# Kernel optimization log

Measured on AMD Instinct MI355X. Metric: run time of the kernel, lower is better.

The kernel has to match this reference:

```python
import jax, jax.numpy as jnp
import numpy as np

T, B = 256, 64
X_DIM, H_DIM, Z_DIM = 128, 1024, 128


def _lin(k, out_d, in_d):
    return jax.random.normal(k, (out_d, in_d), jnp.float32) * 0.05


def setup_inputs() -> dict:
    key = jax.random.key(0)
    ks = jax.random.split(key, 18)
    return {
        "x": jax.random.normal(ks[0], (T, B, X_DIM), jnp.float32),
        "y": jax.random.uniform(ks[1], (T, B, X_DIM), jnp.float32),
        "eps": jax.random.normal(ks[2], (T, B, Z_DIM), jnp.float32),
        # hidden_state_rnn: GRU(x_dim -> h_dim), bias=False
        "h_Wih": _lin(ks[3], 3 * H_DIM, X_DIM),
        "h_Whh": _lin(ks[4], 3 * H_DIM, H_DIM),
        # rnn: GRU(h_dim + x_dim -> h_dim), bias=False (input is [y_t, h_t])
        "a_Wih": _lin(ks[5], 3 * H_DIM, X_DIM + H_DIM),
        "a_Whh": _lin(ks[6], 3 * H_DIM, H_DIM),
        "enc_W1": _lin(ks[7], H_DIM, H_DIM), "enc_b1": jnp.zeros(H_DIM, jnp.float32),
        "enc_W2": _lin(ks[8], H_DIM, H_DIM), "enc_b2": jnp.zeros(H_DIM, jnp.float32),
        "encm_W": _lin(ks[9], Z_DIM, H_DIM), "encm_b": jnp.zeros(Z_DIM, jnp.float32),
        "encs_W": _lin(ks[10], Z_DIM, H_DIM), "encs_b": jnp.zeros(Z_DIM, jnp.float32),
        "pr_W": _lin(ks[11], H_DIM, H_DIM), "pr_b": jnp.zeros(H_DIM, jnp.float32),
        "prm_W": _lin(ks[12], Z_DIM, H_DIM), "prm_b": jnp.zeros(Z_DIM, jnp.float32),
        "prs_W": _lin(ks[13], Z_DIM, H_DIM), "prs_b": jnp.zeros(Z_DIM, jnp.float32),
        "dec_W1": _lin(ks[14], H_DIM, H_DIM + Z_DIM), "dec_b1": jnp.zeros(H_DIM, jnp.float32),
        "dec_W2": _lin(ks[15], H_DIM, H_DIM), "dec_b2": jnp.zeros(H_DIM, jnp.float32),
        "decm_W": _lin(ks[16], X_DIM, H_DIM), "decm_b": jnp.zeros(X_DIM, jnp.float32),
        "decs_W": _lin(ks[17], X_DIM, H_DIM), "decs_b": jnp.zeros(X_DIM, jnp.float32),
    }


def _gru(xs, Wih, Whh):
    """Single-layer PyTorch-style GRU without biases. xs: [T,B,in]. Returns [T,B,H]."""
    h0 = jnp.zeros((xs.shape[1], Whh.shape[1]), xs.dtype)
    def step(h, xt):
        gi = xt @ Wih.T                      # [B, 3H]
        gh = h @ Whh.T                       # [B, 3H]
        ir, iz, inn = jnp.split(gi, 3, axis=-1)
        hr, hz, hn = jnp.split(gh, 3, axis=-1)
        r = jax.nn.sigmoid(ir + hr)
        zg = jax.nn.sigmoid(iz + hz)
        n = jnp.tanh(inn + r * hn)
        h_new = (1.0 - zg) * n + zg * h
        return h_new, h_new
    return jax.lax.scan(step, h0, xs)[1]


def srnn_forward(x, y, eps, h_Wih, h_Whh, a_Wih, a_Whh,
                 enc_W1, enc_b1, enc_W2, enc_b2, encm_W, encm_b, encs_W, encs_b,
                 pr_W, pr_b, prm_W, prm_b, prs_W, prs_b,
                 dec_W1, dec_b1, dec_W2, dec_b2, decm_W, decm_b, decs_W, decs_b):
    h_seq = _gru(x, h_Wih, h_Whh)            # [T,B,H] forward-time states
    # NOTE: original code aliases h_list and reverses it in place, so all later
    # uses of h_list[t] actually see the time-reversed sequence. Reproduce that.
    h_rev = h_seq[::-1]
    y_rev = y[::-1]
    a_rev = _gru(jnp.concatenate([y_rev, h_rev], axis=-1), a_Wih, a_Whh)  # backward GRU
    a_fwd = a_rev[::-1]                      # a at forward time t saw steps t..T-1

    enc = jax.nn.relu(jax.nn.relu(a_fwd @ enc_W1.T + enc_b1) @ enc_W2.T + enc_b2)
    enc_mean = enc @ encm_W.T + encm_b       # [T,B,Z]
    enc_std = jax.nn.softplus(enc @ encs_W.T + encs_b)
    z = eps * enc_std + enc_mean             # reparameterized sample

    pri = jax.nn.relu(h_rev @ pr_W.T + pr_b)  # bug-faithful: reversed h
    prior_mean = pri @ prm_W.T + prm_b
    prior_std = jax.nn.softplus(pri @ prs_W.T + prs_b)

    dec = jax.nn.relu(
        jax.nn.relu(jnp.concatenate([z, h_rev], axis=-1) @ dec_W1.T + dec_b1)
        @ dec_W2.T + dec_b2)
    dec_mean = jax.nn.sigmoid(dec @ decm_W.T + decm_b)  # [T,B,X]
    dec_std = jax.nn.softplus(dec @ decs_W.T + decs_b)

    kld = 0.5 * jnp.sum(
        2.0 * jnp.log(prior_std) - 2.0 * jnp.log(enc_std)
        + (enc_std ** 2 + (enc_mean - prior_mean) ** 2) / prior_std ** 2 - 1.0)
    nll = -jnp.sum(y * jnp.log(dec_mean) + (1.0 - y) * jnp.log(1.0 - dec_mean))
    return kld, nll, enc_mean, enc_std, dec_mean, dec_std


def reference(x, y, eps, h_Wih, h_Whh, a_Wih, a_Whh,
              enc_W1, enc_b1, enc_W2, enc_b2, encm_W, encm_b, encs_W, encs_b,
              pr_W, pr_b, prm_W, prm_b, prs_W, prs_b,
              dec_W1, dec_b1, dec_W2, dec_b2, decm_W, decm_b, decs_W, decs_b):
    return srnn_forward(x, y, eps, h_Wih, h_Whh, a_Wih, a_Whh,
                        enc_W1, enc_b1, enc_W2, enc_b2, encm_W, encm_b, encs_W, encs_b,
                        pr_W, pr_b, prm_W, prm_b, prs_W, prs_b,
                        dec_W1, dec_b1, dec_W2, dec_b2, decm_W, decm_b, decs_W, decs_b)
```

## Files before the change

### kernel.cpp

```cpp
#include <hip/hip_runtime.h>
#include <cstdint>
#include <cstddef>

#define NT   256
#define NB   64
#define XD   128
#define HD   1024
#define ZD   128
#define H3   3072
#define TBM  16384

typedef __attribute__((ext_vector_type(8))) short bf16x8;
typedef __attribute__((ext_vector_type(4))) float f32x4;
typedef __attribute__((ext_vector_type(4))) unsigned int u32x4;

__device__ __forceinline__ unsigned short f2bf(float f){
  unsigned int u = __float_as_uint(f);
  u += 0x7fffu + ((u >> 16) & 1u);
  return (unsigned short)(u >> 16);
}
__device__ __forceinline__ float bf2f(unsigned short h){
  return __uint_as_float(((unsigned int)h) << 16);
}

template<int N>
__device__ __forceinline__ void vwait(){
  asm volatile("s_waitcnt vmcnt(%0)" :: "i"(N) : "memory");
  __builtin_amdgcn_sched_barrier(0);
}

__device__ __forceinline__ float fsigmoid(float x){
  return 1.f / (1.f + __expf(-x));
}
__device__ __forceinline__ float ftanh(float x){
  float xc = fminf(fmaxf(x, -15.f), 15.f);
  float e = __expf(2.f * xc);
  return (e - 1.f) / (e + 1.f);
}

__device__ __forceinline__ void wait_tags(const unsigned int* tags, unsigned int target){
  if (threadIdx.x < 64){
    const unsigned int* p = tags + threadIdx.x * 32;
    unsigned int a, b;
    asm volatile("global_load_dword %0, %2, off sc0 sc1\n\t"
                 "global_load_dword %1, %2, off sc0 sc1"
                 : "=v"(a), "=v"(b) : "v"(p) : "memory");
    for (;;){
      asm volatile("s_waitcnt vmcnt(1)" ::: "memory");
      __builtin_amdgcn_sched_barrier(0);
      if (__all((int)(a >= target))) break;
      asm volatile("global_load_dword %0, %1, off sc0 sc1" : "=v"(a) : "v"(p) : "memory");
      asm volatile("s_waitcnt vmcnt(1)" ::: "memory");
      __builtin_amdgcn_sched_barrier(0);
      if (__all((int)(b >= target))) break;
      asm volatile("global_load_dword %0, %1, off sc0 sc1" : "=v"(b) : "v"(p) : "memory");
    }
    asm volatile("s_waitcnt vmcnt(0)" ::: "memory");
    __builtin_amdgcn_sched_barrier(0);
  }
  __syncthreads();
}

struct CvtArgs { const float* src[17]; };

__global__ void cvt_all(CvtArgs a, unsigned short* wdst, unsigned short* xdst, unsigned short* ydst){
  const long NG = 2572288;
  for (long g = blockIdx.x*blockDim.x + threadIdx.x; g < NG; g += (long)gridDim.x*blockDim.x){
    long i = g * 8;
    const float* s; unsigned short* d;
    if      (i < 393216)  { s=a.src[0]+i;             d=wdst+i; }
    else if (i < 3538944) { s=a.src[1]+(i-393216);    d=wdst+i; }
    else if (i < 7077888) { s=a.src[2]+(i-3538944);   d=wdst+i; }
    else if (i < 10223616){ s=a.src[3]+(i-7077888);   d=wdst+i; }
    else if (i < 11272192){ s=a.src[4]+(i-10223616);  d=wdst+i; }
    else if (i < 12320768){ s=a.src[5]+(i-11272192);  d=wdst+i; }
    else if (i < 12451840){ s=a.src[6]+(i-12320768);  d=wdst+i; }
    else if (i < 12582912){ s=a.src[7]+(i-12451840);  d=wdst+i; }
    else if (i < 13631488){ s=a.src[8]+(i-12582912);  d=wdst+i; }
    else if (i < 13762560){ s=a.src[9]+(i-13631488);  d=wdst+i; }
    else if (i < 13893632){ s=a.src[10]+(i-13762560); d=wdst+i; }
    else if (i < 15073280){ s=a.src[11]+(i-13893632); d=wdst+i; }
    else if (i < 16121856){ s=a.src[12]+(i-15073280); d=wdst+i; }
    else if (i < 16252928){ s=a.src[13]+(i-16121856); d=wdst+i; }
    else if (i < 16384000){ s=a.src[14]+(i-16252928); d=wdst+i; }
    else if (i < 18481152){ s=a.src[15]+(i-16384000); d=xdst+(i-16384000); }
    else                  { s=a.src[16]+(i-18481152); d=ydst+(i-18481152); }
    float4 v0 = *(const float4*)s;
    float4 v1 = *(const float4*)(s + 4);
    u32x4 o;
    o.x = (unsigned int)f2bf(v0.x) | ((unsigned int)f2bf(v0.y) << 16);
    o.y = (unsigned int)f2bf(v0.z) | ((unsigned int)f2bf(v0.w) << 16);
    o.z = (unsigned int)f2bf(v1.x) | ((unsigned int)f2bf(v1.y) << 16);
    o.w = (unsigned int)f2bf(v1.z) | ((unsigned int)f2bf(v1.w) << 16);
    *(u32x4*)d = o;
  }
}

template<int ACT, int OUT_BF, int BIAS>
__launch_bounds__(256)
__global__ void gemm_bf16(const unsigned short* __restrict__ A1, int rev1, int K1,
                          const unsigned short* __restrict__ A2, int rev2, int K,
                          const unsigned short* __restrict__ W,
                          const float* __restrict__ bias,
                          void* __restrict__ Cv, int N, int m0)
{
  __shared__ __align__(16) unsigned short As[128][40];
  __shared__ __align__(16) unsigned short Ws[128][40];
  const int tid   = threadIdx.x;
  const int mbase = blockIdx.y * 128;
  const int nbase = blockIdx.x * 128;
  const int wid = tid >> 6, lane = tid & 63;
  const int wr = wid >> 1, wc = wid & 1;
  const int fr = lane & 15;
  const int kc = (lane >> 4) * 8;
  const int K2 = K - K1;
  const int nk = K >> 5;

  f32x4 acc[4][4];
  #pragma unroll
  for (int i = 0; i < 4; ++i)
    #pragma unroll
    for (int j = 0; j < 4; ++j)
      acc[i][j] = (f32x4){0.f, 0.f, 0.f, 0.f};

  for (int ks = 0; ks < nk; ++ks){
    const int k0 = ks << 5;
    __syncthreads();
    for (int l = tid; l < 512; l += 256){
      int row = l >> 2, c = l & 3;
      int kk = k0 + c*8;
      int m = m0 + mbase + row;
      uint4 v;
      if (kk < K1){
        int mm = rev1 ? (((255 - (m >> 6)) << 6) | (m & 63)) : m;
        v = *(const uint4*)(A1 + (size_t)mm * K1 + kk);
      } else {
        int mm = rev2 ? (((255 - (m >> 6)) << 6) | (m & 63)) : m;
        v = *(const uint4*)(A2 + (size_t)mm * K2 + (kk - K1));
      }
      *(uint4*)&As[row][c*8] = v;
    }
    for (int l = tid; l < 512; l += 256){
      int row = l >> 2, c = l & 3;
      uint4 v = *(const uint4*)(W + (size_t)(nbase + row) * K + k0 + c*8);
      *(uint4*)&Ws[row][c*8] = v;
    }
    __syncthreads();
    bf16x8 af[4], bfm[4];
    #pragma unroll
    for (int f = 0; f < 4; ++f) af[f]  = *(const bf16x8*)&As[wr*64 + f*16 + fr][kc];
    #pragma unroll
    for (int f = 0; f < 4; ++f) bfm[f] = *(const bf16x8*)&Ws[wc*64 + f*16 + fr][kc];
    #pragma unroll
    for (int i = 0; i < 4; ++i)
      #pragma unroll
      for (int j = 0; j < 4; ++j)
        acc[i][j] = __builtin_amdgcn_mfma_f32_16x16x32_bf16(af[i], bfm[j], acc[i][j], 0, 0, 0);
  }

  #pragma unroll
  for (int i = 0; i < 4; ++i){
    #pragma unroll
    for (int j = 0; j < 4; ++j){
      #pragma unroll
      for (int r = 0; r < 4; ++r){
        int row = mbase + wr*64 + i*16 + (lane >> 4)*4 + r;
        int col = nbase + wc*64 + j*16 + fr;
        float v = acc[i][j][r];
        if (BIAS) v += bias[col];
        if (ACT == 1) v = fmaxf(v, 0.f);
        else if (ACT == 2) v = 1.f / (1.f + expf(-v));
        else if (ACT == 3) v = (v > 20.f) ? v : log1pf(expf(v));
        if (OUT_BF) ((unsigned short*)Cv)[(size_t)row * N + col] = f2bf(v);
        else        ((float*)Cv)[(size_t)row * N + col] = v;
      }
    }
  }
}

template<int ACTA, int ACTB>
__launch_bounds__(256)
__global__ void gemm_dual(const unsigned short* __restrict__ A,
                          const unsigned short* __restrict__ Wa, const float* __restrict__ ba,
                          float* __restrict__ Ca,
                          const unsigned short* __restrict__ Wb, const float* __restrict__ bb,
                          float* __restrict__ Cb)
{
  const unsigned short* W = blockIdx.x ? Wb : Wa;
  const float* bias = blockIdx.x ? bb : ba;
  float* C = blockIdx.x ? Cb : Ca;
  const int act = blockIdx.x ? ACTB : ACTA;

  __shared__ __align__(16) unsigned short As[128][40];
  __shared__ __align__(16) unsigned short Ws[128][40];
  const int tid   = threadIdx.x;
  const int mbase = blockIdx.y * 128;
  const int wid = tid >> 6, lane = tid & 63;
  const int wr = wid >> 1, wc = wid & 1;
  const int fr = lane & 15;
  const int kc = (lane >> 4) * 8;

  f32x4 acc[4][4];
  #pragma unroll
  for (int i = 0; i < 4; ++i)
    #pragma unroll
    for (int j = 0; j < 4; ++j)
      acc[i][j] = (f32x4){0.f, 0.f, 0.f, 0.f};

  for (int ks = 0; ks < 32; ++ks){
    const int k0 = ks << 5;
    __syncthreads();
    for (int l = tid; l < 512; l += 256){
      int row = l >> 2, c = l & 3;
      *(uint4*)&As[row][c*8] = *(const uint4*)(A + (size_t)(mbase + row) * HD + k0 + c*8);
    }
    for (int l = tid; l < 512; l += 256){
      int row = l >> 2, c = l & 3;
      *(uint4*)&Ws[row][c*8] = *(const uint4*)(W + (size_t)row * HD + k0 + c*8);
    }
    __syncthreads();
    bf16x8 af[4], bfm[4];
    #pragma unroll
    for (int f = 0; f < 4; ++f) af[f]  = *(const bf16x8*)&As[wr*64 + f*16 + fr][kc];
    #pragma unroll
    for (int f = 0; f < 4; ++f) bfm[f] = *(const bf16x8*)&Ws[wc*64 + f*16 + fr][kc];
    #pragma unroll
    for (int i = 0; i < 4; ++i)
      #pragma unroll
      for (int j = 0; j < 4; ++j)
        acc[i][j] = __builtin_amdgcn_mfma_f32_16x16x32_bf16(af[i], bfm[j], acc[i][j], 0, 0, 0);
  }

  #pragma unroll
  for (int i = 0; i < 4; ++i){
    #pragma unroll
    for (int j = 0; j < 4; ++j){
      #pragma unroll
      for (int r = 0; r < 4; ++r){
        int row = mbase + wr*64 + i*16 + (lane >> 4)*4 + r;
        int col = wc*64 + j*16 + fr;
        float v = acc[i][j][r] + bias[col];
        if (act == 1) v = fmaxf(v, 0.f);
        else if (act == 2) v = 1.f / (1.f + expf(-v));
        else if (act == 3) v = (v > 20.f) ? v : log1pf(expf(v));
        C[(size_t)row * ZD + col] = v;
      }
    }
  }
}

__device__ void gemm_gi_tile(char* smem,
                             const unsigned short* __restrict__ A1, int rev1, int K1,
                             const unsigned short* __restrict__ A2, int rev2, int K,
                             const unsigned short* __restrict__ W,
                             unsigned short* __restrict__ C, int m0, int bx, int by)
{
  unsigned short (*As)[40] = (unsigned short(*)[40])smem;
  unsigned short (*Ws)[40] = (unsigned short(*)[40])(smem + 10240);
  const int tid   = threadIdx.x;
  const int mbase = by * 128;
  const int nbase = bx * 128;
  const int wid = tid >> 6, lane = tid & 63;
  const int wr = wid >> 1, wc = wid & 1;
  const int fr = lane & 15;
  const int kc = (lane >> 4) * 8;
  const int K2 = K - K1;
  const int nk = K >> 5;

  f32x4 acc[4][4];
  #pragma unroll
  for (int i = 0; i < 4; ++i)
    #pragma unroll
    for (int j = 0; j < 4; ++j)
      acc[i][j] = (f32x4){0.f, 0.f, 0.f, 0.f};

  for (int ks = 0; ks < nk; ++ks){
    const int k0 = ks << 5;
    __syncthreads();
    for (int l = tid; l < 512; l += 256){
      int row = l >> 2, c = l & 3;
      int kk = k0 + c*8;
      int m = m0 + mbase + row;
      uint4 v;
      if (kk < K1){
        int mm = rev1 ? (((255 - (m >> 6)) << 6) | (m & 63)) : m;
        v = *(const uint4*)(A1 + (size_t)mm * K1 + kk);
      } else {
        int mm = rev2 ? (((255 - (m >> 6)) << 6) | (m & 63)) : m;
        v = *(const uint4*)(A2 + (size_t)mm * K2 + (kk - K1));
      }
      *(uint4*)&As[row][c*8] = v;
    }
    for (int l = tid; l < 512; l += 256){
      int row = l >> 2, c = l & 3;
      uint4 v = *(const uint4*)(W + (size_t)(nbase + row) * K + k0 + c*8);
      *(uint4*)&Ws[row][c*8] = v;
    }
    __syncthreads();
    bf16x8 af[4], bfm[4];
    #pragma unroll
    for (int f = 0; f < 4; ++f) af[f]  = *(const bf16x8*)&As[wr*64 + f*16 + fr][kc];
    #pragma unroll
    for (int f = 0; f < 4; ++f) bfm[f] = *(const bf16x8*)&Ws[wc*64 + f*16 + fr][kc];
    #pragma unroll
    for (int i = 0; i < 4; ++i)
      #pragma unroll
      for (int j = 0; j < 4; ++j)
        acc[i][j] = __builtin_amdgcn_mfma_f32_16x16x32_bf16(af[i], bfm[j], acc[i][j], 0, 0, 0);
  }

  #pragma unroll
  for (int i = 0; i < 4; ++i){
    #pragma unroll
    for (int j = 0; j < 4; ++j){
      #pragma unroll
      for (int r = 0; r < 4; ++r){
        int row = mbase + wr*64 + i*16 + (lane >> 4)*4 + r;
        int col = nbase + wc*64 + j*16 + fr;
        C[(size_t)row * H3 + col] = f2bf(acc[i][j][r]);
      }
    }
  }
  __syncthreads();
}

__device__ void gru_body(char* smem,
                         const unsigned short* __restrict__ W3,
                         const unsigned short* __restrict__ gi,
                         unsigned short* __restrict__ seq,
                         float* __restrict__ hstate,
                         unsigned int* __restrict__ tags,
                         int t0, int dir, int out_off, int nsteps)
{
  uint4 (*Wf)[3][64] = (uint4(*)[3][64])smem;
  unsigned short (*hb2)[16] = (unsigned short(*)[16])(smem + 98304);
  const int tid  = threadIdx.x;
  const int bid  = blockIdx.x;
  const int c0   = bid * 16;
  const int wid  = tid >> 6, lane = tid & 63;
  const int fr   = lane & 15, q = lane >> 4;
  const int rowb = wid*16 + q*4;
  const int arow = wid*16 + fr;

  for (int ks = wid*8; ks < wid*8 + 8; ++ks)
    #pragma unroll
    for (int g = 0; g < 3; ++g)
      Wf[ks][g][lane] = *(const uint4*)(W3 + (size_t)(g*HD + c0 + fr)*HD + ks*32 + q*8);

  float hc[4];
  if (t0 == 0){
    hc[0] = hc[1] = hc[2] = hc[3] = 0.f;
  } else {
    #pragma unroll
    for (int r = 0; r < 4; ++r)
      hc[r] = hstate[(size_t)(rowb + r)*HD + c0 + fr];
  }
  __syncthreads();

  for (int tt = 0; tt < nsteps; ++tt){
    const int t = t0 + tt;

    unsigned short g_ir[4], g_iz[4], g_in[4];
    {
      const unsigned short* gb = gi + (size_t)tt*NB*H3;
      #pragma unroll
      for (int r = 0; r < 4; ++r){
        const unsigned short* p = gb + (size_t)(rowb + r)*H3 + c0 + fr;
        g_ir[r] = p[0];
        g_iz[r] = p[HD];
        g_in[r] = p[2*HD];
      }
    }

    f32x4 aR = (f32x4){0.f,0.f,0.f,0.f};
    f32x4 aZ = (f32x4){0.f,0.f,0.f,0.f};
    f32x4 aN = (f32x4){0.f,0.f,0.f,0.f};

    if (t > 0){
      if (tt >= 1) wait_tags(tags, (unsigned int)tt);
      const unsigned short* hp = seq + (size_t)(out_off + dir*(t-1))*NB*HD
                                     + (size_t)arow*HD + q*8;
      u32x4 A[32];
      #pragma unroll
      for (int ks = 0; ks < 32; ++ks)
        asm volatile("global_load_dwordx4 %0, %1, off offset:%2"
                     : "=v"(A[ks]) : "v"(hp), "i"(ks*64));
      #pragma unroll
      for (int b4 = 0; b4 < 4; ++b4){
        if (b4 == 0) vwait<24>();
        else if (b4 == 1) vwait<16>();
        else if (b4 == 2) vwait<8>();
        else vwait<0>();
        #pragma unroll
        for (int k8 = 0; k8 < 8; ++k8){
          const int ks = b4*8 + k8;
          bf16x8 a = *(const bf16x8*)&A[ks];
          aR = __builtin_amdgcn_mfma_f32_16x16x32_bf16(a, *(const bf16x8*)&Wf[ks][0][lane], aR, 0, 0, 0);
          aZ = __builtin_amdgcn_mfma_f32_16x16x32_bf16(a, *(const bf16x8*)&Wf[ks][1][lane], aZ, 0, 0, 0);
          aN = __builtin_amdgcn_mfma_f32_16x16x32_bf16(a, *(const bf16x8*)&Wf[ks][2][lane], aN, 0, 0, 0);
        }
      }
    }

    #pragma unroll
    for (int r = 0; r < 4; ++r){
      float rr = fsigmoid(bf2f(g_ir[r]) + aR[r]);
      float zz = fsigmoid(bf2f(g_iz[r]) + aZ[r]);
      float nn = ftanh(bf2f(g_in[r]) + rr * aN[r]);
      hc[r] = (1.f - zz) * nn + zz * hc[r];
      hb2[rowb + r][fr] = f2bf(hc[r]);
    }
    __syncthreads();
    {
      int row = tid >> 2, c4 = (tid & 3) * 4;
      unsigned long long v = *(const unsigned long long*)&hb2[row][c4];
      unsigned long long* dst = (unsigned long long*)(seq + (size_t)(out_off + dir*t)*NB*HD
                                                          + (size_t)row*HD + c0 + c4);
      (void)__hip_atomic_exchange(dst, v, __ATOMIC_RELAXED, __HIP_MEMORY_SCOPE_AGENT);
    }
    if (tt < nsteps - 1){
      vwait<0>();
      __syncthreads();
      if (tid == 0)
        (void)__hip_atomic_exchange(tags + bid*32, (unsigned int)(tt + 1),
                                    __ATOMIC_RELAXED, __HIP_MEMORY_SCOPE_AGENT);
    }
  }

  #pragma unroll
  for (int r = 0; r < 4; ++r)
    hstate[(size_t)(rowb + r)*HD + c0 + fr] = hc[r];
}

__global__ __launch_bounds__(256, 1)
void gru_seq(const unsigned short* __restrict__ W3, const unsigned short* __restrict__ gi,
             unsigned short* __restrict__ seq, float* __restrict__ hstate,
             unsigned int* __restrict__ tags, int t0, int dir, int out_off, int nsteps)
{
  __shared__ __align__(16) char smem[100608];
  gru_body(smem, W3, gi, seq, hstate, tags, t0, dir, out_off, nsteps);
}

__global__ __launch_bounds__(256, 1)
void gru_fat(const unsigned short* __restrict__ W3, const unsigned short* __restrict__ gi,
             unsigned short* __restrict__ seq, float* __restrict__ hstate,
             unsigned int* __restrict__ tags, int t0, int dir, int out_off, int nsteps,
             const unsigned short* __restrict__ gA1, int grev1, int gK1,
             const unsigned short* __restrict__ gA2, int grev2, int gK,
             const unsigned short* __restrict__ gW, unsigned short* __restrict__ gC, int gm0)
{
  __shared__ __align__(16) char smem[100608];
  if (blockIdx.x < 64){
    gru_body(smem, W3, gi, seq, hstate, tags, t0, dir, out_off, nsteps);
  } else {
    for (int tl = blockIdx.x - 64; tl < 768; tl += 96)
      gemm_gi_tile(smem, gA1, grev1, gK1, gA2, grev2, gK, gW, gC, gm0, tl % 24, tl / 24);
  }
}

__global__ void z_make(const float* __restrict__ eps, const float* __restrict__ em,
                       const float* __restrict__ es, unsigned short* __restrict__ zb, int n){
  for (int i = blockIdx.x*blockDim.x + threadIdx.x; i < n; i += gridDim.x*blockDim.x)
    zb[i] = f2bf(eps[i] * es[i] + em[i]);
}

__global__ void kld_partial(const float* __restrict__ em, const float* __restrict__ es,
                            const float* __restrict__ pm, const float* __restrict__ ps,
                            float* __restrict__ part, int n){
  float s = 0.f;
  for (int i = blockIdx.x*blockDim.x + threadIdx.x; i < n; i += gridDim.x*blockDim.x){
    float e = es[i], p = ps[i], d = em[i] - pm[i];
    s += 2.f*(logf(p) - logf(e)) + (e*e + d*d)/(p*p) - 1.f;
  }
  __shared__ float red[256];
  red[threadIdx.x] = s; __syncthreads();
  for (int off = 128; off; off >>= 1){
    if (threadIdx.x < off) red[threadIdx.x] += red[threadIdx.x + off];
    __syncthreads();
  }
  if (threadIdx.x == 0) part[blockIdx.x] = red[0];
}

__global__ void nll_partial(const float* __restrict__ y, const float* __restrict__ dm,
                            float* __restrict__ part, int n){
  float s = 0.f;
  for (int i = blockIdx.x*blockDim.x + threadIdx.x; i < n; i += gridDim.x*blockDim.x){
    float yy = y[i], d = dm[i];
    s += yy * logf(d) + (1.f - yy) * logf(1.f - d);
  }
  __shared__ float red[256];
  red[threadIdx.x] = s; __syncthreads();
  for (int off = 128; off; off >>= 1){
    if (threadIdx.x < off) red[threadIdx.x] += red[threadIdx.x + off];
    __syncthreads();
  }
  if (threadIdx.x == 0) part[blockIdx.x] = red[0];
}

__global__ void final_sum(const float* __restrict__ part, int n, float scale, float* __restrict__ out){
  float s = 0.f;
  for (int i = threadIdx.x; i < n; i += 256) s += part[i];
  __shared__ float red[256];
  red[threadIdx.x] = s; __syncthreads();
  for (int off = 128; off; off >>= 1){
    if (threadIdx.x < off) red[threadIdx.x] += red[threadIdx.x + off];
    __syncthreads();
  }
  if (threadIdx.x == 0) out[0] = scale * red[0];
}

extern "C" void kernel_launch(void* const* d_in, const int* in_sizes, int n_in,
                              void* d_out, int out_size, void* d_ws, size_t ws_size,
                              hipStream_t stream)
{
  const float* y   = (const float*)d_in[1];
  const float* eps = (const float*)d_in[2];
  const float* enc_b1 = (const float*)d_in[8];
  const float* enc_b2 = (const float*)d_in[10];
  const float* encm_b = (const float*)d_in[12];
  const float* encs_b = (const float*)d_in[14];
  const float* pr_b   = (const float*)d_in[16];
  const float* prm_b  = (const float*)d_in[18];
  const float* prs_b  = (const float*)d_in[20];
  const float* dec_b1 = (const float*)d_in[22];
  const float* dec_b2 = (const float*)d_in[24];
  const float* decm_b = (const float*)d_in[26];
  const float* decs_b = (const float*)d_in[28];

  char* ws = (char*)d_ws;
  size_t off = 0;
  auto alloc = [&](size_t bytes){ size_t o = off; off += (bytes + 255) & ~(size_t)255; return o; };
  const size_t o_big   = alloc((size_t)71303168);
  const size_t o_hseq  = alloc((size_t)TBM * HD * 2);
  const size_t o_aseq  = alloc((size_t)TBM * HD * 2);
  const size_t o_wbf   = alloc((size_t)16384000 * 2);
  const size_t o_hst   = alloc((size_t)NB * HD * 4);
  const size_t o_bar   = alloc((size_t)65536);
  const size_t o_pkld  = alloc((size_t)1024 * 4);
  const size_t o_pnll  = alloc((size_t)1024 * 4);
  (void)off; (void)ws_size;

  char* big = ws + o_big;
  unsigned short* gihA = (unsigned short*)(big);
  unsigned short* gihB = (unsigned short*)(big + 25165824);
  unsigned short* xbf  = (unsigned short*)(big + 50331648);
  unsigned short* ybf  = (unsigned short*)(big + 54525952);
  unsigned short* tA  = (unsigned short*)(big);
  unsigned short* tB  = (unsigned short*)(big + 33554432);
  unsigned short* zbf = (unsigned short*)(big + 67108864);

  unsigned short* hseq = (unsigned short*)(ws + o_hseq);
  unsigned short* aseq = (unsigned short*)(ws + o_aseq);
  unsigned short* wbf  = (unsigned short*)(ws + o_wbf);
  float* hstate = (float*)(ws + o_hst);
  unsigned int* bar = (unsigned int*)(ws + o_bar);
  float* pkld = (float*)(ws + o_pkld);
  float* pnll = (float*)(ws + o_pnll);

  const int widx[15] = {3,4,5,6,7,9,11,13,15,17,19,21,23,25,27};
  const size_t wsz[15] = {393216,3145728,3538944,3145728,1048576,1048576,131072,131072,
                          1048576,131072,131072,1179648,1048576,131072,131072};
  size_t woff[15]; { size_t a = 0; for (int i = 0; i < 15; ++i){ woff[i] = a; a += wsz[i]; } }
  unsigned short* w_hWih = wbf + woff[0];
  unsigned short* w_hWhh = wbf + woff[1];
  unsigned short* w_aWih = wbf + woff[2];
  unsigned short* w_aWhh = wbf + woff[3];
  unsigned short* w_enc1 = wbf + woff[4];
  unsigned short* w_enc2 = wbf + woff[5];
  unsigned short* w_encm = wbf + woff[6];
  unsigned short* w_encs = wbf + woff[7];
  unsigned short* w_pr   = wbf + woff[8];
  unsigned short* w_prm  = wbf + woff[9];
  unsigned short* w_prs  = wbf + woff[10];
  unsigned short* w_dec1 = wbf + woff[11];
  unsigned short* w_dec2 = wbf + woff[12];
  unsigned short* w_decm = wbf + woff[13];
  unsigned short* w_decs = wbf + woff[14];

  float* out = (float*)d_out;
  float* em_out = out + 2;
  float* es_out = out + 2 + 2097152;
  float* dm_out = out + 2 + 2*2097152;
  float* ds_out = out + 2 + 3*2097152;
  float* pm = dm_out;
  float* ps = ds_out;

  CvtArgs ca;
  for (int i = 0; i < 15; ++i) ca.src[i] = (const float*)d_in[widx[i]];
  ca.src[15] = (const float*)d_in[0];
  ca.src[16] = (const float*)d_in[1];
  cvt_all<<<2048, 256, 0, stream>>>(ca, wbf, xbf, ybf);
  (void)hipMemsetAsync(bar, 0, 65536, stream);

  const dim3 blk(256);
  const dim3 gQ3072(24, 32);
  const dim3 g1024(HD/128, TBM/128);
  const dim3 gDual(2, TBM/128);
  const unsigned short* nul = (const unsigned short*)nullptr;

  gemm_bf16<0,1,0><<<gQ3072, blk, 0, stream>>>(xbf, 0, XD, nul, 0, XD, w_hWih, nullptr, gihA, H3, 0);
  gru_fat<<<160, blk, 0, stream>>>(w_hWhh, gihA, hseq, hstate, bar + 0*2048, 0,   +1, 0, 64,
                                   xbf, 0, XD, nul, 0, XD, w_hWih, gihB, 4096);
  gru_fat<<<160, blk, 0, stream>>>(w_hWhh, gihB, hseq, hstate, bar + 1*2048, 64,  +1, 0, 64,
                                   xbf, 0, XD, nul, 0, XD, w_hWih, gihA, 8192);
  gru_fat<<<160, blk, 0, stream>>>(w_hWhh, gihA, hseq, hstate, bar + 2*2048, 128, +1, 0, 64,
                                   xbf, 0, XD, nul, 0, XD, w_hWih, gihB, 12288);
  gru_seq<<<64, blk, 0, stream>>>(w_hWhh, gihB, hseq, hstate, bar + 3*2048, 192, +1, 0, 64);

  gemm_bf16<0,1,0><<<gQ3072, blk, 0, stream>>>(ybf, 1, XD, hseq, 1, XD + HD, w_aWih, nullptr, gihA, H3, 0);
  gru_fat<<<160, blk, 0, stream>>>(w_aWhh, gihA, aseq, hstate, bar + 4*2048, 0,   -1, 255, 64,
                                   ybf, 1, XD, hseq, 1, XD + HD, w_aWih, gihB, 4096);
  gru_fat<<<160, blk, 0, stream>>>(w_aWhh, gihB, aseq, hstate, bar + 5*2048, 64,  -1, 255, 64,
                                   ybf, 1, XD, hseq, 1, XD + HD, w_aWih, gihA, 8192);
  gru_fat<<<160, blk, 0, stream>>>(w_aWhh, gihA, aseq, hstate, bar + 6*2048, 128, -1, 255, 64,
                                   ybf, 1, XD, hseq, 1, XD + HD, w_aWih, gihB, 12288);
  gru_seq<<<64, blk, 0, stream>>>(w_aWhh, gihB, aseq, hstate, bar + 7*2048, 192, -1, 255, 64);

  gemm_bf16<1,1,1><<<g1024, blk, 0, stream>>>(aseq, 0, HD, nul, 0, HD, w_enc1, enc_b1, tA, HD, 0);
  gemm_bf16<1,1,1><<<g1024, blk, 0, stream>>>(tA, 0, HD, nul, 0, HD, w_enc2, enc_b2, tB, HD, 0);
  gemm_dual<0,3><<<gDual, blk, 0, stream>>>(tB, w_encm, encm_b, em_out, w_encs, encs_b, es_out);
  z_make<<<2048, 256, 0, stream>>>(eps, em_out, es_out, zbf, TBM*ZD);

  gemm_bf16<1,1,1><<<g1024, blk, 0, stream>>>(hseq, 1, HD, nul, 1, HD, w_pr, pr_b, tA, HD, 0);
  gemm_dual<0,3><<<gDual, blk, 0, stream>>>(tA, w_prm, prm_b, pm, w_prs, prs_b, ps);
  kld_partial<<<1024, 256, 0, stream>>>(em_out, es_out, pm, ps, pkld, TBM*ZD);
  final_sum<<<1, 256, 0, stream>>>(pkld, 1024, 0.5f, out + 0);

  gemm_bf16<1,1,1><<<g1024, blk, 0, stream>>>(zbf, 0, ZD, hseq, 1, ZD + HD, w_dec1, dec_b1, tA, HD, 0);
  gemm_bf16<1,1,1><<<g1024, blk, 0, stream>>>(tA, 0, HD, nul, 0, HD, w_dec2, dec_b2, tB, HD, 0);
  gemm_dual<2,3><<<gDual, blk, 0, stream>>>(tB, w_decm, decm_b, dm_out, w_decs, decs_b, ds_out);

  nll_partial<<<1024, 256, 0, stream>>>(y, dm_out, pnll, TBM*XD);
  final_sum<<<1, 256, 0, stream>>>(pnll, 1024, -1.0f, out + 1);
}
```

Before: 4.633 ms.

## Fuse mean/std head GEMMs with z sampling, KLD and NLL reductions; per-wave barrier tags

```diff
diff --git a/kernel.cpp b/kernel.cpp
--- a/kernel.cpp
+++ b/kernel.cpp
@@ -41,19 +41,19 @@
 __device__ __forceinline__ void wait_tags(const unsigned int* tags, unsigned int target){
   if (threadIdx.x < 64){
     const unsigned int* p = tags + threadIdx.x * 32;
-    unsigned int a, b;
-    asm volatile("global_load_dword %0, %2, off sc0 sc1\n\t"
-                 "global_load_dword %1, %2, off sc0 sc1"
+    u32x4 a, b;
+    asm volatile("global_load_dwordx4 %0, %2, off sc0 sc1\n\t"
+                 "global_load_dwordx4 %1, %2, off sc0 sc1"
                  : "=v"(a), "=v"(b) : "v"(p) : "memory");
     for (;;){
       asm volatile("s_waitcnt vmcnt(1)" ::: "memory");
       __builtin_amdgcn_sched_barrier(0);
-      if (__all((int)(a >= target))) break;
-      asm volatile("global_load_dword %0, %1, off sc0 sc1" : "=v"(a) : "v"(p) : "memory");
+      if (__all((int)(a.x >= target && a.y >= target && a.z >= target && a.w >= target))) break;
+      asm volatile("global_load_dwordx4 %0, %1, off sc0 sc1" : "=v"(a) : "v"(p) : "memory");
       asm volatile("s_waitcnt vmcnt(1)" ::: "memory");
       __builtin_amdgcn_sched_barrier(0);
-      if (__all((int)(b >= target))) break;
-      asm volatile("global_load_dword %0, %1, off sc0 sc1" : "=v"(b) : "v"(p) : "memory");
+      if (__all((int)(b.x >= target && b.y >= target && b.z >= target && b.w >= target))) break;
+      asm volatile("global_load_dwordx4 %0, %1, off sc0 sc1" : "=v"(b) : "v"(p) : "memory");
     }
     asm volatile("s_waitcnt vmcnt(0)" ::: "memory");
     __builtin_amdgcn_sched_barrier(0);
@@ -178,74 +178,105 @@
   }
 }
 
-template<int ACTA, int ACTB>
+template<int MODE>
 __launch_bounds__(256)
-__global__ void gemm_dual(const unsigned short* __restrict__ A,
-                          const unsigned short* __restrict__ Wa, const float* __restrict__ ba,
-                          float* __restrict__ Ca,
-                          const unsigned short* __restrict__ Wb, const float* __restrict__ bb,
-                          float* __restrict__ Cb)
+__global__ void gemm_two(const unsigned short* __restrict__ A,
+                         const unsigned short* __restrict__ Wa, const float* __restrict__ ba,
+                         const unsigned short* __restrict__ Wb, const float* __restrict__ bb,
+                         float* __restrict__ Oa, float* __restrict__ Ob,
+                         const float* __restrict__ aux1, const float* __restrict__ aux2,
+                         unsigned short* __restrict__ zb, float* __restrict__ part)
 {
-  const unsigned short* W = blockIdx.x ? Wb : Wa;
-  const float* bias = blockIdx.x ? bb : ba;
-  float* C = blockIdx.x ? Cb : Ca;
-  const int act = blockIdx.x ? ACTB : ACTA;
-
   __shared__ __align__(16) unsigned short As[128][40];
-  __shared__ __align__(16) unsigned short Ws[128][40];
+  __shared__ __align__(16) unsigned short Wsa[128][40];
+  __shared__ __align__(16) unsigned short Wsb[128][40];
+  __shared__ float red[256];
   const int tid   = threadIdx.x;
-  const int mbase = blockIdx.y * 128;
+  const int mbase = blockIdx.x * 128;
   const int wid = tid >> 6, lane = tid & 63;
   const int wr = wid >> 1, wc = wid & 1;
-  const int fr = lane & 15;
-  const int kc = (lane >> 4) * 8;
-
-  f32x4 acc[4][4];
+  const int fr = lane & 15, q = lane >> 4;
+  const int kc = q * 8;
+
+  f32x4 accA[4][4], accB[4][4];
   #pragma unroll
   for (int i = 0; i < 4; ++i)
     #pragma unroll
-    for (int j = 0; j < 4; ++j)
-      acc[i][j] = (f32x4){0.f, 0.f, 0.f, 0.f};
+    for (int j = 0; j < 4; ++j){
+      accA[i][j] = (f32x4){0.f, 0.f, 0.f, 0.f};
+      accB[i][j] = (f32x4){0.f, 0.f, 0.f, 0.f};
+    }
 
   for (int ks = 0; ks < 32; ++ks){
     const int k0 = ks << 5;
     __syncthreads();
     for (int l = tid; l < 512; l += 256){
       int row = l >> 2, c = l & 3;
-      *(uint4*)&As[row][c*8] = *(const uint4*)(A + (size_t)(mbase + row) * HD + k0 + c*8);
+      *(uint4*)&As[row][c*8]  = *(const uint4*)(A  + (size_t)(mbase + row) * HD + k0 + c*8);
     }
     for (int l = tid; l < 512; l += 256){
       int row = l >> 2, c = l & 3;
-      *(uint4*)&Ws[row][c*8] = *(const uint4*)(W + (size_t)row * HD + k0 + c*8);
-    }
-    __syncthreads();
-    bf16x8 af[4], bfm[4];
-    #pragma unroll
-    for (int f = 0; f < 4; ++f) af[f]  = *(const bf16x8*)&As[wr*64 + f*16 + fr][kc];
-    #pragma unroll
-    for (int f = 0; f < 4; ++f) bfm[f] = *(const bf16x8*)&Ws[wc*64 + f*16 + fr][kc];
+      *(uint4*)&Wsa[row][c*8] = *(const uint4*)(Wa + (size_t)row * HD + k0 + c*8);
+    }
+    for (int l = tid; l < 512; l += 256){
+      int row = l >> 2, c = l & 3;
+      *(uint4*)&Wsb[row][c*8] = *(const uint4*)(Wb + (size_t)row * HD + k0 + c*8);
+    }
+    __syncthreads();
+    bf16x8 af[4], wa[4], wb[4];
+    #pragma unroll
+    for (int f = 0; f < 4; ++f) af[f] = *(const bf16x8*)&As[wr*64 + f*16 + fr][kc];
+    #pragma unroll
+    for (int f = 0; f < 4; ++f) wa[f] = *(const bf16x8*)&Wsa[wc*64 + f*16 + fr][kc];
+    #pragma unroll
+    for (int f = 0; f < 4; ++f) wb[f] = *(const bf16x8*)&Wsb[wc*64 + f*16 + fr][kc];
     #pragma unroll
     for (int i = 0; i < 4; ++i)
       #pragma unroll
-      for (int j = 0; j < 4; ++j)
-        acc[i][j] = __builtin_amdgcn_mfma_f32_16x16x32_bf16(af[i], bfm[j], acc[i][j], 0, 0, 0);
-  }
-
+      for (int j = 0; j < 4; ++j){
+        accA[i][j] = __builtin_amdgcn_mfma_f32_16x16x32_bf16(af[i], wa[j], accA[i][j], 0, 0, 0);
+        accB[i][j] = __builtin_amdgcn_mfma_f32_16x16x32_bf16(af[i], wb[j], accB[i][j], 0, 0, 0);
+      }
+  }
+
+  float s = 0.f;
   #pragma unroll
   for (int i = 0; i < 4; ++i){
     #pragma unroll
     for (int j = 0; j < 4; ++j){
       #pragma unroll
       for (int r = 0; r < 4; ++r){
-        int row = mbase + wr*64 + i*16 + (lane >> 4)*4 + r;
+        int row = mbase + wr*64 + i*16 + q*4 + r;
         int col = wc*64 + j*16 + fr;
-        float v = acc[i][j][r] + bias[col];
-        if (act == 1) v = fmaxf(v, 0.f);
-        else if (act == 2) v = 1.f / (1.f + expf(-v));
-        else if (act == 3) v = (v > 20.f) ? v : log1pf(expf(v));
-        C[(size_t)row * ZD + col] = v;
-      }
-    }
+        size_t idx = (size_t)row * ZD + col;
+        float va = accA[i][j][r] + ba[col];
+        float vb = accB[i][j][r] + bb[col];
+        float sb = (vb > 20.f) ? vb : log1pf(expf(vb));
+        if (MODE == 0){
+          Oa[idx] = va;
+          Ob[idx] = sb;
+          zb[idx] = f2bf(aux1[idx] * sb + va);
+        } else if (MODE == 1){
+          float em = aux1[idx], es = aux2[idx];
+          float d = em - va;
+          s += 2.f*(logf(sb) - logf(es)) + (es*es + d*d)/(sb*sb) - 1.f;
+        } else {
+          float dm = 1.f / (1.f + expf(-va));
+          Oa[idx] = dm;
+          Ob[idx] = sb;
+          float yy = aux1[idx];
+          s += yy * logf(dm) + (1.f - yy) * logf(1.f - dm);
+        }
+      }
+    }
+  }
+  if (MODE != 0){
+    red[tid] = s; __syncthreads();
+    for (int off2 = 128; off2; off2 >>= 1){
+      if (tid < off2) red[tid] += red[tid + off2];
+      __syncthreads();
+    }
+    if (tid == 0) part[blockIdx.x] = red[0];
   }
 }
 
@@ -420,9 +451,8 @@
     }
     if (tt < nsteps - 1){
       vwait<0>();
-      __syncthreads();
-      if (tid == 0)
-        (void)__hip_atomic_exchange(tags + bid*32, (unsigned int)(tt + 1),
+      if (lane == 0)
+        (void)__hip_atomic_exchange(tags + bid*32 + wid, (unsigned int)(tt + 1),
                                     __ATOMIC_RELAXED, __HIP_MEMORY_SCOPE_AGENT);
     }
   }
@@ -456,45 +486,6 @@
     for (int tl = blockIdx.x - 64; tl < 768; tl += 96)
       gemm_gi_tile(smem, gA1, grev1, gK1, gA2, grev2, gK, gW, gC, gm0, tl % 24, tl / 24);
   }
-}
-
-__global__ void z_make(const float* __restrict__ eps, const float* __restrict__ em,
-                       const float* __restrict__ es, unsigned short* __restrict__ zb, int n){
-  for (int i = blockIdx.x*blockDim.x + threadIdx.x; i < n; i += gridDim.x*blockDim.x)
-    zb[i] = f2bf(eps[i] * es[i] + em[i]);
-}
-
-__global__ void kld_partial(const float* __restrict__ em, const float* __restrict__ es,
-                            const float* __restrict__ pm, const float* __restrict__ ps,
-                            float* __restrict__ part, int n){
-  float s = 0.f;
-  for (int i = blockIdx.x*blockDim.x + threadIdx.x; i < n; i += gridDim.x*blockDim.x){
-    float e = es[i], p = ps[i], d = em[i] - pm[i];
-    s += 2.f*(logf(p) - logf(e)) + (e*e + d*d)/(p*p) - 1.f;
-  }
-  __shared__ float red[256];
-  red[threadIdx.x] = s; __syncthreads();
-  for (int off = 128; off; off >>= 1){
-    if (threadIdx.x < off) red[threadIdx.x] += red[threadIdx.x + off];
-    __syncthreads();
-  }
-  if (threadIdx.x == 0) part[blockIdx.x] = red[0];
-}
-
-__global__ void nll_partial(const float* __restrict__ y, const float* __restrict__ dm,
-                            float* __restrict__ part, int n){
-  float s = 0.f;
-  for (int i = blockIdx.x*blockDim.x + threadIdx.x; i < n; i += gridDim.x*blockDim.x){
-    float yy = y[i], d = dm[i];
-    s += yy * logf(d) + (1.f - yy) * logf(1.f - d);
-  }
-  __shared__ float red[256];
-  red[threadIdx.x] = s; __syncthreads();
-  for (int off = 128; off; off >>= 1){
-    if (threadIdx.x < off) red[threadIdx.x] += red[threadIdx.x + off];
-    __syncthreads();
-  }
-  if (threadIdx.x == 0) part[blockIdx.x] = red[0];
 }
 
 __global__ void final_sum(const float* __restrict__ part, int n, float scale, float* __restrict__ out){
@@ -582,8 +573,6 @@
   float* es_out = out + 2 + 2097152;
   float* dm_out = out + 2 + 2*2097152;
   float* ds_out = out + 2 + 3*2097152;
-  float* pm = dm_out;
-  float* ps = ds_out;
 
   CvtArgs ca;
   for (int i = 0; i < 15; ++i) ca.src[i] = (const float*)d_in[widx[i]];
@@ -595,7 +584,6 @@
   const dim3 blk(256);
   const dim3 gQ3072(24, 32);
   const dim3 g1024(HD/128, TBM/128);
-  const dim3 gDual(2, TBM/128);
   const unsigned short* nul = (const unsigned short*)nullptr;
 
   gemm_bf16<0,1,0><<<gQ3072, blk, 0, stream>>>(xbf, 0, XD, nul, 0, XD, w_hWih, nullptr, gihA, H3, 0);
@@ -618,18 +606,17 @@
 
   gemm_bf16<1,1,1><<<g1024, blk, 0, stream>>>(aseq, 0, HD, nul, 0, HD, w_enc1, enc_b1, tA, HD, 0);
   gemm_bf16<1,1,1><<<g1024, blk, 0, stream>>>(tA, 0, HD, nul, 0, HD, w_enc2, enc_b2, tB, HD, 0);
-  gemm_dual<0,3><<<gDual, blk, 0, stream>>>(tB, w_encm, encm_b, em_out, w_encs, encs_b, es_out);
-  z_make<<<2048, 256, 0, stream>>>(eps, em_out, es_out, zbf, TBM*ZD);
+  gemm_two<0><<<128, blk, 0, stream>>>(tB, w_encm, encm_b, w_encs, encs_b,
+                                       em_out, es_out, eps, nullptr, zbf, nullptr);
 
   gemm_bf16<1,1,1><<<g1024, blk, 0, stream>>>(hseq, 1, HD, nul, 1, HD, w_pr, pr_b, tA, HD, 0);
-  gemm_dual<0,3><<<gDual, blk, 0, stream>>>(tA, w_prm, prm_b, pm, w_prs, prs_b, ps);
-  kld_partial<<<1024, 256, 0, stream>>>(em_out, es_out, pm, ps, pkld, TBM*ZD);
-  final_sum<<<1, 256, 0, stream>>>(pkld, 1024, 0.5f, out + 0);
+  gemm_two<1><<<128, blk, 0, stream>>>(tA, w_prm, prm_b, w_prs, prs_b,
+                                       nullptr, nullptr, em_out, es_out, nullptr, pkld);
+  final_sum<<<1, 256, 0, stream>>>(pkld, 128, 0.5f, out + 0);
 
   gemm_bf16<1,1,1><<<g1024, blk, 0, stream>>>(zbf, 0, ZD, hseq, 1, ZD + HD, w_dec1, dec_b1, tA, HD, 0);
   gemm_bf16<1,1,1><<<g1024, blk, 0, stream>>>(tA, 0, HD, nul, 0, HD, w_dec2, dec_b2, tB, HD, 0);
-  gemm_dual<2,3><<<gDual, blk, 0, stream>>>(tB, w_decm, decm_b, dm_out, w_decs, decs_b, ds_out);
-
-  nll_partial<<<1024, 256, 0, stream>>>(y, dm_out, pnll, TBM*XD);
-  final_sum<<<1, 256, 0, stream>>>(pnll, 1024, -1.0f, out + 1);
-}
+  gemm_two<2><<<128, blk, 0, stream>>>(tB, w_decm, decm_b, w_decs, decs_b,
+                                       dm_out, ds_out, y, nullptr, nullptr, pnll);
+  final_sum<<<1, 256, 0, stream>>>(pnll, 128, -1.0f, out + 1);
+}
```

Result: slower. 5.005 ms (+8.0%).
